# Kernel tuning notes

Measured on AMD Instinct MI355X. Metric: run time of the kernel, lower is better.

## Reference

```python
import jax, jax.numpy as jnp
import numpy as np

N_NODES = 100000
N_EDGES = 640000
N_FEAT = 128


def setup_inputs() -> dict:
    key = jax.random.key(0)
    k1, k2, k3, k4 = jax.random.split(key, 4)
    x = jax.random.normal(k1, (N_NODES, N_FEAT), dtype=jnp.float32)
    edge_index = jax.random.randint(k2, (2, N_EDGES), 0, N_NODES, dtype=jnp.int32)
    # Glorot-ish init for weights
    W_conv = jax.random.normal(k3, (N_FEAT, N_FEAT), dtype=jnp.float32) / np.sqrt(N_FEAT)
    b_conv = jnp.zeros((N_FEAT,), dtype=jnp.float32)
    W_lin = jax.random.normal(k4, (1, N_FEAT), dtype=jnp.float32) / np.sqrt(N_FEAT)
    b_lin = jnp.zeros((1,), dtype=jnp.float32)
    return {"x": x, "edge_index": edge_index, "W_conv": W_conv,
            "b_conv": b_conv, "W_lin": W_lin, "b_lin": b_lin}


def gcn_conv(x, edge_index, W, b):
    # PyG GCNConv: add self-loops, symmetric normalization D^-1/2 (A+I) D^-1/2,
    # linear transform first (no bias in lin), bias added after aggregation.
    N = x.shape[0]
    loop = jnp.arange(N, dtype=edge_index.dtype)
    src = jnp.concatenate([edge_index[0], loop])  # [E+N]
    dst = jnp.concatenate([edge_index[1], loop])  # [E+N]
    deg = jax.ops.segment_sum(jnp.ones_like(dst, dtype=x.dtype), dst, num_segments=N)
    dinv = jnp.where(deg > 0, jax.lax.rsqrt(deg), 0.0)
    norm = dinv[src] * dinv[dst]                   # [E+N]
    xw = x @ W.T                                   # [N, F]
    msg = xw[src] * norm[:, None]                  # [E+N, F] gather + scale
    agg = jax.ops.segment_sum(msg, dst, num_segments=N)  # scatter-add
    return agg + b


def reference(x, edge_index, W_conv, b_conv, W_lin, b_lin):
    h = jax.nn.relu(gcn_conv(x, edge_index, W_conv, b_conv))
    out = jax.nn.sigmoid(h @ W_lin.T + b_lin)
    return (out, h)
```

## Files before the change

### kernel.cpp

```cpp
#include <hip/hip_runtime.h>
#include <hip/hip_bf16.h>

#define NN 100000
#define NE 640000
#define NF 128
#define CAP 32
#define ECAP 36
#define LDW 136
#define EBLK 625
#define XBLK 6250
#define WBLK 8

typedef short bf16x8 __attribute__((ext_vector_type(8)));
typedef float f32x4  __attribute__((ext_vector_type(4)));

__device__ __forceinline__ unsigned short f2bf(float f) {
    union { float f; unsigned int i; } v; v.f = f;
    unsigned int x = v.i;
    return (unsigned short)((x + 0x7FFFu + ((x >> 16) & 1u)) >> 16);
}

__global__ void k_zero(int* __restrict__ fill) {
    int i = blockIdx.x * blockDim.x + threadIdx.x;
    if (i < NN / 4) *(int4*)(fill + i * 4) = (int4){0, 0, 0, 0};
}

__global__ void k_build(const float* __restrict__ x, const float* __restrict__ W,
                        const int* __restrict__ src, const int* __restrict__ dst,
                        int* __restrict__ fill, int* __restrict__ esrc,
                        unsigned short* __restrict__ xs,
                        unsigned short* __restrict__ wb) {
    int b = blockIdx.x;
    if (b < EBLK) {
        int e = (b * 256 + threadIdx.x) * 4;
        int4 s4 = *(const int4*)(src + e);
        int4 d4 = *(const int4*)(dst + e);
        int p0 = atomicAdd(&fill[d4.x], 1);
        int p1 = atomicAdd(&fill[d4.y], 1);
        int p2 = atomicAdd(&fill[d4.z], 1);
        int p3 = atomicAdd(&fill[d4.w], 1);
        if (p0 < CAP) esrc[(long)d4.x * CAP + p0] = s4.x;
        if (p1 < CAP) esrc[(long)d4.y * CAP + p1] = s4.y;
        if (p2 < CAP) esrc[(long)d4.z * CAP + p2] = s4.z;
        if (p3 < CAP) esrc[(long)d4.w * CAP + p3] = s4.w;
    } else if (b < EBLK + XBLK) {
        int t = (b - EBLK) * 256 + threadIdx.x;
        int node = t >> 4, fc = (t & 15) * 8;
        const float* xp = x + (long)node * NF + fc;
        float4 a = *(const float4*)(xp);
        float4 c = *(const float4*)(xp + 4);
        int4 u;
        u.x = (unsigned)f2bf(a.x) | ((unsigned)f2bf(a.y) << 16);
        u.y = (unsigned)f2bf(a.z) | ((unsigned)f2bf(a.w) << 16);
        u.z = (unsigned)f2bf(c.x) | ((unsigned)f2bf(c.y) << 16);
        u.w = (unsigned)f2bf(c.z) | ((unsigned)f2bf(c.w) << 16);
        *(int4*)(xs + (long)node * NF + fc) = u;
    } else {
        int t = (b - EBLK - XBLK) * 256 + threadIdx.x;
        int idx = t * 8;
        float4 a = *(const float4*)(W + idx);
        float4 c = *(const float4*)(W + idx + 4);
        int4 u;
        u.x = (unsigned)f2bf(a.x) | ((unsigned)f2bf(a.y) << 16);
        u.y = (unsigned)f2bf(a.z) | ((unsigned)f2bf(a.w) << 16);
        u.z = (unsigned)f2bf(c.x) | ((unsigned)f2bf(c.y) << 16);
        u.w = (unsigned)f2bf(c.z) | ((unsigned)f2bf(c.w) << 16);
        *(int4*)(wb + idx) = u;
    }
}

__device__ __forceinline__ void acc_row_s(float* acc, int4 u, float s) {
    acc[0] = fmaf(s, __int_as_float((unsigned)u.x << 16), acc[0]);
    acc[1] = fmaf(s, __int_as_float(u.x & 0xffff0000), acc[1]);
    acc[2] = fmaf(s, __int_as_float((unsigned)u.y << 16), acc[2]);
    acc[3] = fmaf(s, __int_as_float(u.y & 0xffff0000), acc[3]);
    acc[4] = fmaf(s, __int_as_float((unsigned)u.z << 16), acc[4]);
    acc[5] = fmaf(s, __int_as_float(u.z & 0xffff0000), acc[5]);
    acc[6] = fmaf(s, __int_as_float((unsigned)u.w << 16), acc[6]);
    acc[7] = fmaf(s, __int_as_float(u.w & 0xffff0000), acc[7]);
}

__launch_bounds__(256, 4)
__global__ void k_fused(const unsigned short* __restrict__ xs,
                        const int* __restrict__ fill,
                        const int* __restrict__ esrc,
                        const unsigned short* __restrict__ wb,
                        const float* __restrict__ bconv,
                        const float* __restrict__ wlin,
                        const float* __restrict__ blin,
                        float* __restrict__ out,
                        float* __restrict__ hout) {
    __shared__ unsigned short lds_a[32 * LDW];
    __shared__ int lds_e[32 * ECAP];
    __shared__ float lds_dv[32];
    __shared__ int lds_dg[32];
    __shared__ float sh_head[2][32];
    int t = threadIdx.x;
    int row0 = blockIdx.x * 32;

    {
        int r = t >> 3, col = (t & 7) * 4;
        *(int4*)(lds_e + r * ECAP + col) =
            *(const int4*)(esrc + (long)(row0 + r) * CAP + col);
    }
    if (t < 32) {
        int dg = fill[row0 + t];
        lds_dv[t] = rsqrtf((float)(dg + 1));
        lds_dg[t] = (dg > CAP) ? CAP : dg;
    }
    __syncthreads();

    {
        int lane = t & 15, slot = t >> 4;
        int fc = lane * 8;
        for (int m = 0; m < 2; ++m) {
            int r = m * 16 + slot;
            int node = row0 + r;
            float dv = lds_dv[r];
            int degc = lds_dg[r];
            const int* ep = lds_e + r * ECAP;

            float acc[8];
            {
                int4 us = *(const int4*)(xs + (long)node * NF + fc);
                acc[0] = dv * __int_as_float((unsigned)us.x << 16);
                acc[1] = dv * __int_as_float(us.x & 0xffff0000);
                acc[2] = dv * __int_as_float((unsigned)us.y << 16);
                acc[3] = dv * __int_as_float(us.y & 0xffff0000);
                acc[4] = dv * __int_as_float((unsigned)us.z << 16);
                acc[5] = dv * __int_as_float(us.z & 0xffff0000);
                acc[6] = dv * __int_as_float((unsigned)us.w << 16);
                acc[7] = dv * __int_as_float(us.w & 0xffff0000);
            }

            for (int j = 0; j < degc; j += 8) {
                int i0 = (j + 0 < degc) ? ep[j + 0] : node;
                int i1 = (j + 1 < degc) ? ep[j + 1] : node;
                int i2 = (j + 2 < degc) ? ep[j + 2] : node;
                int i3 = (j + 3 < degc) ? ep[j + 3] : node;
                int i4 = (j + 4 < degc) ? ep[j + 4] : node;
                int i5 = (j + 5 < degc) ? ep[j + 5] : node;
                int i6 = (j + 6 < degc) ? ep[j + 6] : node;
                int i7 = (j + 7 < degc) ? ep[j + 7] : node;
                int f0 = fill[i0], f1 = fill[i1];
                int f2 = fill[i2], f3 = fill[i3];
                int f4 = fill[i4], f5 = fill[i5];
                int f6 = fill[i6], f7 = fill[i7];
                int4 v0 = *(const int4*)(xs + (long)i0 * NF + fc);
                int4 v1 = *(const int4*)(xs + (long)i1 * NF + fc);
                int4 v2 = *(const int4*)(xs + (long)i2 * NF + fc);
                int4 v3 = *(const int4*)(xs + (long)i3 * NF + fc);
                int4 v4 = *(const int4*)(xs + (long)i4 * NF + fc);
                int4 v5 = *(const int4*)(xs + (long)i5 * NF + fc);
                int4 v6 = *(const int4*)(xs + (long)i6 * NF + fc);
                int4 v7 = *(const int4*)(xs + (long)i7 * NF + fc);
                float s0 = (j + 0 < degc) ? rsqrtf((float)(f0 + 1)) : 0.f;
                float s1 = (j + 1 < degc) ? rsqrtf((float)(f1 + 1)) : 0.f;
                float s2 = (j + 2 < degc) ? rsqrtf((float)(f2 + 1)) : 0.f;
                float s3 = (j + 3 < degc) ? rsqrtf((float)(f3 + 1)) : 0.f;
                float s4 = (j + 4 < degc) ? rsqrtf((float)(f4 + 1)) : 0.f;
                float s5 = (j + 5 < degc) ? rsqrtf((float)(f5 + 1)) : 0.f;
                float s6 = (j + 6 < degc) ? rsqrtf((float)(f6 + 1)) : 0.f;
                float s7 = (j + 7 < degc) ? rsqrtf((float)(f7 + 1)) : 0.f;
                acc_row_s(acc, v0, s0); acc_row_s(acc, v1, s1);
                acc_row_s(acc, v2, s2); acc_row_s(acc, v3, s3);
                acc_row_s(acc, v4, s4); acc_row_s(acc, v5, s5);
                acc_row_s(acc, v6, s6); acc_row_s(acc, v7, s7);
            }

            int4 st;
            st.x = (unsigned)f2bf(acc[0] * dv) | ((unsigned)f2bf(acc[1] * dv) << 16);
            st.y = (unsigned)f2bf(acc[2] * dv) | ((unsigned)f2bf(acc[3] * dv) << 16);
            st.z = (unsigned)f2bf(acc[4] * dv) | ((unsigned)f2bf(acc[5] * dv) << 16);
            st.w = (unsigned)f2bf(acc[6] * dv) | ((unsigned)f2bf(acc[7] * dv) << 16);
            *(int4*)(lds_a + r * LDW + fc) = st;
        }
    }
    __syncthreads();

    int w = t >> 6, lane = t & 63;
    int quad = lane >> 4, nr = lane & 15;
    int mrow = (w >> 1) * 16;
    int ncol0 = (w & 1) * 64;
    int kq = quad * 8;

    f32x4 acc4[4];
#pragma unroll
    for (int nt = 0; nt < 4; ++nt) acc4[nt] = (f32x4){0.f, 0.f, 0.f, 0.f};

#pragma unroll
    for (int ks = 0; ks < 4; ++ks) {
        bf16x8 af = *(const bf16x8*)(lds_a + (mrow + nr) * LDW + ks * 32 + kq);
#pragma unroll
        for (int nt = 0; nt < 4; ++nt) {
            bf16x8 bf = *(const bf16x8*)(wb + (ncol0 + nt * 16 + nr) * NF + ks * 32 + kq);
            acc4[nt] = __builtin_amdgcn_mfma_f32_16x16x32_bf16(af, bf, acc4[nt], 0, 0, 0);
        }
    }

    float bcv[4], wlv[4];
#pragma unroll
    for (int nt = 0; nt < 4; ++nt) {
        int col = ncol0 + nt * 16 + nr;
        bcv[nt] = bconv[col];
        wlv[nt] = wlin[col];
    }
    float p[4] = {0.f, 0.f, 0.f, 0.f};
#pragma unroll
    for (int nt = 0; nt < 4; ++nt) {
        int col = ncol0 + nt * 16 + nr;
#pragma unroll
        for (int r = 0; r < 4; ++r) {
            float h = fmaxf(acc4[nt][r] + bcv[nt], 0.0f);
            int row = row0 + mrow + quad * 4 + r;
            hout[(long)row * NF + col] = h;
            p[r] += h * wlv[nt];
        }
    }
#pragma unroll
    for (int r = 0; r < 4; ++r) {
#pragma unroll
        for (int off = 1; off <= 8; off <<= 1)
            p[r] += __shfl_xor(p[r], off, 64);
        if (nr == 0) sh_head[w & 1][mrow + quad * 4 + r] = p[r];
    }
    __syncthreads();
    if (t < 32) {
        float z = sh_head[0][t] + sh_head[1][t] + blin[0];
        out[row0 + t] = 1.0f / (1.0f + expf(-z));
    }
}

extern "C" void kernel_launch(void* const* d_in, const int* in_sizes, int n_in,
                              void* d_out, int out_size, void* d_ws, size_t ws_size,
                              hipStream_t stream) {
    const float* x     = (const float*)d_in[0];
    const int*   ei    = (const int*)d_in[1];
    const float* Wc    = (const float*)d_in[2];
    const float* bconv = (const float*)d_in[3];
    const float* wlin  = (const float*)d_in[4];
    const float* blin  = (const float*)d_in[5];
    const int* src = ei;
    const int* dst = ei + NE;

    float* out  = (float*)d_out;
    float* hout = out + NN;

    int*            esrc = (int*)d_ws;
    unsigned short* xs   = (unsigned short*)(esrc + (size_t)NN * CAP);
    unsigned short* wb   = xs + (size_t)NN * NF;
    int*            fill = (int*)(wb + NF * NF);

    k_zero <<<(NN / 4 + 255) / 256, 256, 0, stream>>>(fill);
    k_build<<<EBLK + XBLK + WBLK, 256, 0, stream>>>(x, Wc, src, dst,
                                                    fill, esrc, xs, wb);
    k_fused<<<NN / 32, 256, 0, stream>>>(xs, fill, esrc, wb,
                                         bconv, wlin, blin, out, hout);
}
```

Before: 200.9 us.

## Transform features before aggregation; fuse GEMM into build and epilogue into aggregation

The linear transform now runs before aggregation, matching the reference order. The bf16 MFMA GEMM moves into the build kernel, where it runs alongside the edge-bucketing atomics and writes bf16 pre-activations. The aggregation kernel then gathers those transformed rows and applies bias, ReLU, the output head and the sigmoid per row, which removes the LDS staging and the second barrier-heavy GEMM phase. The zero and W-convert steps merge into one init kernel, and edge bucketing goes to one edge per thread. Rounding x@W to bf16 before the sum changes the numerics slightly.

```diff
diff --git a/kernel.cpp b/kernel.cpp
--- a/kernel.cpp
+++ b/kernel.cpp
@@ -7,9 +7,9 @@
 #define CAP 32
 #define ECAP 36
 #define LDW 136
-#define EBLK 625
-#define XBLK 6250
-#define WBLK 8
+#define ABLK 2500
+#define NTILE 3125
+#define NN_PAD 100352
 
 typedef short bf16x8 __attribute__((ext_vector_type(8)));
 typedef float f32x4  __attribute__((ext_vector_type(4)));
@@ -19,44 +19,16 @@
     unsigned int x = v.i;
     return (unsigned short)((x + 0x7FFFu + ((x >> 16) & 1u)) >> 16);
 }
-
-__global__ void k_zero(int* __restrict__ fill) {
-    int i = blockIdx.x * blockDim.x + threadIdx.x;
-    if (i < NN / 4) *(int4*)(fill + i * 4) = (int4){0, 0, 0, 0};
-}
-
-__global__ void k_build(const float* __restrict__ x, const float* __restrict__ W,
-                        const int* __restrict__ src, const int* __restrict__ dst,
-                        int* __restrict__ fill, int* __restrict__ esrc,
-                        unsigned short* __restrict__ xs,
-                        unsigned short* __restrict__ wb) {
-    int b = blockIdx.x;
-    if (b < EBLK) {
-        int e = (b * 256 + threadIdx.x) * 4;
-        int4 s4 = *(const int4*)(src + e);
-        int4 d4 = *(const int4*)(dst + e);
-        int p0 = atomicAdd(&fill[d4.x], 1);
-        int p1 = atomicAdd(&fill[d4.y], 1);
-        int p2 = atomicAdd(&fill[d4.z], 1);
-        int p3 = atomicAdd(&fill[d4.w], 1);
-        if (p0 < CAP) esrc[(long)d4.x * CAP + p0] = s4.x;
-        if (p1 < CAP) esrc[(long)d4.y * CAP + p1] = s4.y;
-        if (p2 < CAP) esrc[(long)d4.z * CAP + p2] = s4.z;
-        if (p3 < CAP) esrc[(long)d4.w * CAP + p3] = s4.w;
-    } else if (b < EBLK + XBLK) {
-        int t = (b - EBLK) * 256 + threadIdx.x;
-        int node = t >> 4, fc = (t & 15) * 8;
-        const float* xp = x + (long)node * NF + fc;
-        float4 a = *(const float4*)(xp);
-        float4 c = *(const float4*)(xp + 4);
-        int4 u;
-        u.x = (unsigned)f2bf(a.x) | ((unsigned)f2bf(a.y) << 16);
-        u.y = (unsigned)f2bf(a.z) | ((unsigned)f2bf(a.w) << 16);
-        u.z = (unsigned)f2bf(c.x) | ((unsigned)f2bf(c.y) << 16);
-        u.w = (unsigned)f2bf(c.z) | ((unsigned)f2bf(c.w) << 16);
-        *(int4*)(xs + (long)node * NF + fc) = u;
+__device__ __forceinline__ float bflo(int u) { return __int_as_float((unsigned)u << 16); }
+__device__ __forceinline__ float bfhi(int u) { return __int_as_float(u & 0xffff0000); }
+
+__global__ void k_init(const float* __restrict__ W, int* __restrict__ fill,
+                       unsigned short* __restrict__ wb) {
+    int i = blockIdx.x * 256 + threadIdx.x;
+    if (i < NN_PAD / 4) {
+        *(int4*)(fill + i * 4) = (int4){0, 0, 0, 0};
     } else {
-        int t = (b - EBLK - XBLK) * 256 + threadIdx.x;
+        int t = i - NN_PAD / 4;
         int idx = t * 8;
         float4 a = *(const float4*)(W + idx);
         float4 c = *(const float4*)(W + idx + 4);
@@ -69,32 +41,81 @@
     }
 }
 
-__device__ __forceinline__ void acc_row_s(float* acc, int4 u, float s) {
-    acc[0] = fmaf(s, __int_as_float((unsigned)u.x << 16), acc[0]);
-    acc[1] = fmaf(s, __int_as_float(u.x & 0xffff0000), acc[1]);
-    acc[2] = fmaf(s, __int_as_float((unsigned)u.y << 16), acc[2]);
-    acc[3] = fmaf(s, __int_as_float(u.y & 0xffff0000), acc[3]);
-    acc[4] = fmaf(s, __int_as_float((unsigned)u.z << 16), acc[4]);
-    acc[5] = fmaf(s, __int_as_float(u.z & 0xffff0000), acc[5]);
-    acc[6] = fmaf(s, __int_as_float((unsigned)u.w << 16), acc[6]);
-    acc[7] = fmaf(s, __int_as_float(u.w & 0xffff0000), acc[7]);
-}
-
 __launch_bounds__(256, 4)
-__global__ void k_fused(const unsigned short* __restrict__ xs,
-                        const int* __restrict__ fill,
-                        const int* __restrict__ esrc,
+__global__ void k_build(const float* __restrict__ x,
+                        const int* __restrict__ src, const int* __restrict__ dst,
+                        int* __restrict__ fill, int* __restrict__ esrc,
                         const unsigned short* __restrict__ wb,
-                        const float* __restrict__ bconv,
-                        const float* __restrict__ wlin,
-                        const float* __restrict__ blin,
-                        float* __restrict__ out,
-                        float* __restrict__ hout) {
+                        unsigned short* __restrict__ hpre) {
     __shared__ unsigned short lds_a[32 * LDW];
+    int bid = blockIdx.x, t = threadIdx.x;
+
+    if (bid < ABLK) {
+        int e = bid * 256 + t;
+        int s = src[e], d = dst[e];
+        int pos = atomicAdd(&fill[d], 1);
+        if (pos < CAP) esrc[(long)d * CAP + pos] = s;
+        return;
+    }
+
+    int row0 = (bid - ABLK) * 32;
+    {
+        int r = t >> 3, cb = (t & 7) * 16;
+        const float* xp = x + (long)(row0 + r) * NF + cb;
+        float4 a = *(const float4*)(xp);
+        float4 b = *(const float4*)(xp + 4);
+        float4 c = *(const float4*)(xp + 8);
+        float4 d = *(const float4*)(xp + 12);
+        int4 u1, u2;
+        u1.x = (unsigned)f2bf(a.x) | ((unsigned)f2bf(a.y) << 16);
+        u1.y = (unsigned)f2bf(a.z) | ((unsigned)f2bf(a.w) << 16);
+        u1.z = (unsigned)f2bf(b.x) | ((unsigned)f2bf(b.y) << 16);
+        u1.w = (unsigned)f2bf(b.z) | ((unsigned)f2bf(b.w) << 16);
+        u2.x = (unsigned)f2bf(c.x) | ((unsigned)f2bf(c.y) << 16);
+        u2.y = (unsigned)f2bf(c.z) | ((unsigned)f2bf(c.w) << 16);
+        u2.z = (unsigned)f2bf(d.x) | ((unsigned)f2bf(d.y) << 16);
+        u2.w = (unsigned)f2bf(d.z) | ((unsigned)f2bf(d.w) << 16);
+        *(int4*)(lds_a + r * LDW + cb) = u1;
+        *(int4*)(lds_a + r * LDW + cb + 8) = u2;
+    }
+    __syncthreads();
+
+    int w = t >> 6, lane = t & 63;
+    int quad = lane >> 4, nr = lane & 15;
+    int mrow = (w >> 1) * 16, ncol0 = (w & 1) * 64, kq = quad * 8;
+
+    f32x4 acc4[4];
+#pragma unroll
+    for (int nt = 0; nt < 4; ++nt) acc4[nt] = (f32x4){0.f, 0.f, 0.f, 0.f};
+#pragma unroll
+    for (int ks = 0; ks < 4; ++ks) {
+        bf16x8 af = *(const bf16x8*)(lds_a + (mrow + nr) * LDW + ks * 32 + kq);
+#pragma unroll
+        for (int nt = 0; nt < 4; ++nt) {
+            bf16x8 bfr = *(const bf16x8*)(wb + (ncol0 + nt * 16 + nr) * NF + ks * 32 + kq);
+            acc4[nt] = __builtin_amdgcn_mfma_f32_16x16x32_bf16(af, bfr, acc4[nt], 0, 0, 0);
+        }
+    }
+#pragma unroll
+    for (int nt = 0; nt < 4; ++nt) {
+        int col = ncol0 + nt * 16 + nr;
+#pragma unroll
+        for (int g = 0; g < 4; ++g)
+            hpre[(long)(row0 + mrow + quad * 4 + g) * NF + col] = f2bf(acc4[nt][g]);
+    }
+}
+
+__launch_bounds__(256, 4)
+__global__ void k_agg(const unsigned short* __restrict__ hpre,
+                      const int* __restrict__ fill,
+                      const int* __restrict__ esrc,
+                      const float* __restrict__ bconv,
+                      const float* __restrict__ wlin,
+                      const float* __restrict__ blin,
+                      float* __restrict__ out, float* __restrict__ hout) {
     __shared__ int lds_e[32 * ECAP];
     __shared__ float lds_dv[32];
     __shared__ int lds_dg[32];
-    __shared__ float sh_head[2][32];
     int t = threadIdx.x;
     int row0 = blockIdx.x * 32;
 
@@ -110,124 +131,108 @@
     }
     __syncthreads();
 
-    {
-        int lane = t & 15, slot = t >> 4;
-        int fc = lane * 8;
-        for (int m = 0; m < 2; ++m) {
-            int r = m * 16 + slot;
-            int node = row0 + r;
-            float dv = lds_dv[r];
-            int degc = lds_dg[r];
-            const int* ep = lds_e + r * ECAP;
-
-            float acc[8];
-            {
-                int4 us = *(const int4*)(xs + (long)node * NF + fc);
-                acc[0] = dv * __int_as_float((unsigned)us.x << 16);
-                acc[1] = dv * __int_as_float(us.x & 0xffff0000);
-                acc[2] = dv * __int_as_float((unsigned)us.y << 16);
-                acc[3] = dv * __int_as_float(us.y & 0xffff0000);
-                acc[4] = dv * __int_as_float((unsigned)us.z << 16);
-                acc[5] = dv * __int_as_float(us.z & 0xffff0000);
-                acc[6] = dv * __int_as_float((unsigned)us.w << 16);
-                acc[7] = dv * __int_as_float(us.w & 0xffff0000);
-            }
-
-            for (int j = 0; j < degc; j += 8) {
-                int i0 = (j + 0 < degc) ? ep[j + 0] : node;
-                int i1 = (j + 1 < degc) ? ep[j + 1] : node;
-                int i2 = (j + 2 < degc) ? ep[j + 2] : node;
-                int i3 = (j + 3 < degc) ? ep[j + 3] : node;
-                int i4 = (j + 4 < degc) ? ep[j + 4] : node;
-                int i5 = (j + 5 < degc) ? ep[j + 5] : node;
-                int i6 = (j + 6 < degc) ? ep[j + 6] : node;
-                int i7 = (j + 7 < degc) ? ep[j + 7] : node;
-                int f0 = fill[i0], f1 = fill[i1];
-                int f2 = fill[i2], f3 = fill[i3];
-                int f4 = fill[i4], f5 = fill[i5];
-                int f6 = fill[i6], f7 = fill[i7];
-                int4 v0 = *(const int4*)(xs + (long)i0 * NF + fc);
-                int4 v1 = *(const int4*)(xs + (long)i1 * NF + fc);
-                int4 v2 = *(const int4*)(xs + (long)i2 * NF + fc);
-                int4 v3 = *(const int4*)(xs + (long)i3 * NF + fc);
-                int4 v4 = *(const int4*)(xs + (long)i4 * NF + fc);
-                int4 v5 = *(const int4*)(xs + (long)i5 * NF + fc);
-                int4 v6 = *(const int4*)(xs + (long)i6 * NF + fc);
-                int4 v7 = *(const int4*)(xs + (long)i7 * NF + fc);
-                float s0 = (j + 0 < degc) ? rsqrtf((float)(f0 + 1)) : 0.f;
-                float s1 = (j + 1 < degc) ? rsqrtf((float)(f1 + 1)) : 0.f;
-                float s2 = (j + 2 < degc) ? rsqrtf((float)(f2 + 1)) : 0.f;
-                float s3 = (j + 3 < degc) ? rsqrtf((float)(f3 + 1)) : 0.f;
-                float s4 = (j + 4 < degc) ? rsqrtf((float)(f4 + 1)) : 0.f;
-                float s5 = (j + 5 < degc) ? rsqrtf((float)(f5 + 1)) : 0.f;
-                float s6 = (j + 6 < degc) ? rsqrtf((float)(f6 + 1)) : 0.f;
-                float s7 = (j + 7 < degc) ? rsqrtf((float)(f7 + 1)) : 0.f;
-                acc_row_s(acc, v0, s0); acc_row_s(acc, v1, s1);
-                acc_row_s(acc, v2, s2); acc_row_s(acc, v3, s3);
-                acc_row_s(acc, v4, s4); acc_row_s(acc, v5, s5);
-                acc_row_s(acc, v6, s6); acc_row_s(acc, v7, s7);
-            }
-
-            int4 st;
-            st.x = (unsigned)f2bf(acc[0] * dv) | ((unsigned)f2bf(acc[1] * dv) << 16);
-            st.y = (unsigned)f2bf(acc[2] * dv) | ((unsigned)f2bf(acc[3] * dv) << 16);
-            st.z = (unsigned)f2bf(acc[4] * dv) | ((unsigned)f2bf(acc[5] * dv) << 16);
-            st.w = (unsigned)f2bf(acc[6] * dv) | ((unsigned)f2bf(acc[7] * dv) << 16);
-            *(int4*)(lds_a + r * LDW + fc) = st;
+    int lane = t & 15, slot = t >> 4;
+    int fc = lane * 8;
+    float bl = blin[0];
+
+    for (int m = 0; m < 2; ++m) {
+        int r = m * 16 + slot;
+        int node = row0 + r;
+        float dv = lds_dv[r];
+        int degc = lds_dg[r];
+        const int* ep = lds_e + r * ECAP;
+
+        float acc[8];
+        {
+            int4 us = *(const int4*)(hpre + (long)node * NF + fc);
+            acc[0] = dv * bflo(us.x); acc[1] = dv * bfhi(us.x);
+            acc[2] = dv * bflo(us.y); acc[3] = dv * bfhi(us.y);
+            acc[4] = dv * bflo(us.z); acc[5] = dv * bfhi(us.z);
+            acc[6] = dv * bflo(us.w); acc[7] = dv * bfhi(us.w);
         }
-    }
-    __syncthreads();
-
-    int w = t >> 6, lane = t & 63;
-    int quad = lane >> 4, nr = lane & 15;
-    int mrow = (w >> 1) * 16;
-    int ncol0 = (w & 1) * 64;
-    int kq = quad * 8;
-
-    f32x4 acc4[4];
-#pragma unroll
-    for (int nt = 0; nt < 4; ++nt) acc4[nt] = (f32x4){0.f, 0.f, 0.f, 0.f};
-
-#pragma unroll
-    for (int ks = 0; ks < 4; ++ks) {
-        bf16x8 af = *(const bf16x8*)(lds_a + (mrow + nr) * LDW + ks * 32 + kq);
-#pragma unroll
-        for (int nt = 0; nt < 4; ++nt) {
-            bf16x8 bf = *(const bf16x8*)(wb + (ncol0 + nt * 16 + nr) * NF + ks * 32 + kq);
-            acc4[nt] = __builtin_amdgcn_mfma_f32_16x16x32_bf16(af, bf, acc4[nt], 0, 0, 0);
+        for (int j = 0; j < degc; j += 8) {
+            int i0 = (j + 0 < degc) ? ep[j + 0] : node;
+            int i1 = (j + 1 < degc) ? ep[j + 1] : node;
+            int i2 = (j + 2 < degc) ? ep[j + 2] : node;
+            int i3 = (j + 3 < degc) ? ep[j + 3] : node;
+            int i4 = (j + 4 < degc) ? ep[j + 4] : node;
+            int i5 = (j + 5 < degc) ? ep[j + 5] : node;
+            int i6 = (j + 6 < degc) ? ep[j + 6] : node;
+            int i7 = (j + 7 < degc) ? ep[j + 7] : node;
+            int f0 = fill[i0], f1 = fill[i1], f2 = fill[i2], f3 = fill[i3];
+            int f4 = fill[i4], f5 = fill[i5], f6 = fill[i6], f7 = fill[i7];
+            int4 v0 = *(const int4*)(hpre + (long)i0 * NF + fc);
+            int4 v1 = *(const int4*)(hpre + (long)i1 * NF + fc);
+            int4 v2 = *(const int4*)(hpre + (long)i2 * NF + fc);
+            int4 v3 = *(const int4*)(hpre + (long)i3 * NF + fc);
+            int4 v4 = *(const int4*)(hpre + (long)i4 * NF + fc);
+            int4 v5 = *(const int4*)(hpre + (long)i5 * NF + fc);
+            int4 v6 = *(const int4*)(hpre + (long)i6 * NF + fc);
+            int4 v7 = *(const int4*)(hpre + (long)i7 * NF + fc);
+            float s0 = (j + 0 < degc) ? rsqrtf((float)(f0 + 1)) : 0.f;
+            float s1 = (j + 1 < degc) ? rsqrtf((float)(f1 + 1)) : 0.f;
+            float s2 = (j + 2 < degc) ? rsqrtf((float)(f2 + 1)) : 0.f;
+            float s3 = (j + 3 < degc) ? rsqrtf((float)(f3 + 1)) : 0.f;
+            float s4 = (j + 4 < degc) ? rsqrtf((float)(f4 + 1)) : 0.f;
+            float s5 = (j + 5 < degc) ? rsqrtf((float)(f5 + 1)) : 0.f;
+            float s6 = (j + 6 < degc) ? rsqrtf((float)(f6 + 1)) : 0.f;
+            float s7 = (j + 7 < degc) ? rsqrtf((float)(f7 + 1)) : 0.f;
+            acc[0] = fmaf(s0, bflo(v0.x), acc[0]); acc[1] = fmaf(s0, bfhi(v0.x), acc[1]);
+            acc[2] = fmaf(s0, bflo(v0.y), acc[2]); acc[3] = fmaf(s0, bfhi(v0.y), acc[3]);
+            acc[4] = fmaf(s0, bflo(v0.z), acc[4]); acc[5] = fmaf(s0, bfhi(v0.z), acc[5]);
+            acc[6] = fmaf(s0, bflo(v0.w), acc[6]); acc[7] = fmaf(s0, bfhi(v0.w), acc[7]);
+            acc[0] = fmaf(s1, bflo(v1.x), acc[0]); acc[1] = fmaf(s1, bfhi(v1.x), acc[1]);
+            acc[2] = fmaf(s1, bflo(v1.y), acc[2]); acc[3] = fmaf(s1, bfhi(v1.y), acc[3]);
+            acc[4] = fmaf(s1, bflo(v1.z), acc[4]); acc[5] = fmaf(s1, bfhi(v1.z), acc[5]);
+            acc[6] = fmaf(s1, bflo(v1.w), acc[6]); acc[7] = fmaf(s1, bfhi(v1.w), acc[7]);
+            acc[0] = fmaf(s2, bflo(v2.x), acc[0]); acc[1] = fmaf(s2, bfhi(v2.x), acc[1]);
+            acc[2] = fmaf(s2, bflo(v2.y), acc[2]); acc[3] = fmaf(s2, bfhi(v2.y), acc[3]);
+            acc[4] = fmaf(s2, bflo(v2.z), acc[4]); acc[5] = fmaf(s2, bfhi(v2.z), acc[5]);
+            acc[6] = fmaf(s2, bflo(v2.w), acc[6]); acc[7] = fmaf(s2, bfhi(v2.w), acc[7]);
+            acc[0] = fmaf(s3, bflo(v3.x), acc[0]); acc[1] = fmaf(s3, bfhi(v3.x), acc[1]);
+            acc[2] = fmaf(s3, bflo(v3.y), acc[2]); acc[3] = fmaf(s3, bfhi(v3.y), acc[3]);
+            acc[4] = fmaf(s3, bflo(v3.z), acc[4]); acc[5] = fmaf(s3, bfhi(v3.z), acc[5]);
+            acc[6] = fmaf(s3, bflo(v3.w), acc[6]); acc[7] = fmaf(s3, bfhi(v3.w), acc[7]);
+            acc[0] = fmaf(s4, bflo(v4.x), acc[0]); acc[1] = fmaf(s4, bfhi(v4.x), acc[1]);
+            acc[2] = fmaf(s4, bflo(v4.y), acc[2]); acc[3] = fmaf(s4, bfhi(v4.y), acc[3]);
+            acc[4] = fmaf(s4, bflo(v4.z), acc[4]); acc[5] = fmaf(s4, bfhi(v4.z), acc[5]);
+            acc[6] = fmaf(s4, bflo(v4.w), acc[6]); acc[7] = fmaf(s4, bfhi(v4.w), acc[7]);
+            acc[0] = fmaf(s5, bflo(v5.x), acc[0]); acc[1] = fmaf(s5, bfhi(v5.x), acc[1]);
+            acc[2] = fmaf(s5, bflo(v5.y), acc[2]); acc[3] = fmaf(s5, bfhi(v5.y), acc[3]);
+            acc[4] = fmaf(s5, bflo(v5.z), acc[4]); acc[5] = fmaf(s5, bfhi(v5.z), acc[5]);
+            acc[6] = fmaf(s5, bflo(v5.w), acc[6]); acc[7] = fmaf(s5, bfhi(v5.w), acc[7]);
+            acc[0] = fmaf(s6, bflo(v6.x), acc[0]); acc[1] = fmaf(s6, bfhi(v6.x), acc[1]);
+            acc[2] = fmaf(s6, bflo(v6.y), acc[2]); acc[3] = fmaf(s6, bfhi(v6.y), acc[3]);
+            acc[4] = fmaf(s6, bflo(v6.z), acc[4]); acc[5] = fmaf(s6, bfhi(v6.z), acc[5]);
+            acc[6] = fmaf(s6, bflo(v6.w), acc[6]); acc[7] = fmaf(s6, bfhi(v6.w), acc[7]);
+            acc[0] = fmaf(s7, bflo(v7.x), acc[0]); acc[1] = fmaf(s7, bfhi(v7.x), acc[1]);
+            acc[2] = fmaf(s7, bflo(v7.y), acc[2]); acc[3] = fmaf(s7, bfhi(v7.y), acc[3]);
+            acc[4] = fmaf(s7, bflo(v7.z), acc[4]); acc[5] = fmaf(s7, bfhi(v7.z), acc[5]);
+            acc[6] = fmaf(s7, bflo(v7.w), acc[6]); acc[7] = fmaf(s7, bfhi(v7.w), acc[7]);
         }
-    }
-
-    float bcv[4], wlv[4];
-#pragma unroll
-    for (int nt = 0; nt < 4; ++nt) {
-        int col = ncol0 + nt * 16 + nr;
-        bcv[nt] = bconv[col];
-        wlv[nt] = wlin[col];
-    }
-    float p[4] = {0.f, 0.f, 0.f, 0.f};
-#pragma unroll
-    for (int nt = 0; nt < 4; ++nt) {
-        int col = ncol0 + nt * 16 + nr;
-#pragma unroll
-        for (int r = 0; r < 4; ++r) {
-            float h = fmaxf(acc4[nt][r] + bcv[nt], 0.0f);
-            int row = row0 + mrow + quad * 4 + r;
-            hout[(long)row * NF + col] = h;
-            p[r] += h * wlv[nt];
-        }
-    }
-#pragma unroll
-    for (int r = 0; r < 4; ++r) {
+
+        float4 bc0 = *(const float4*)(bconv + fc);
+        float4 bc1 = *(const float4*)(bconv + fc + 4);
+        float4 wl0 = *(const float4*)(wlin + fc);
+        float4 wl1 = *(const float4*)(wlin + fc + 4);
+        float4 h0, h1;
+        h0.x = fmaxf(acc[0] * dv + bc0.x, 0.f);
+        h0.y = fmaxf(acc[1] * dv + bc0.y, 0.f);
+        h0.z = fmaxf(acc[2] * dv + bc0.z, 0.f);
+        h0.w = fmaxf(acc[3] * dv + bc0.w, 0.f);
+        h1.x = fmaxf(acc[4] * dv + bc1.x, 0.f);
+        h1.y = fmaxf(acc[5] * dv + bc1.y, 0.f);
+        h1.z = fmaxf(acc[6] * dv + bc1.z, 0.f);
+        h1.w = fmaxf(acc[7] * dv + bc1.w, 0.f);
+        *(float4*)(hout + (long)node * NF + fc) = h0;
+        *(float4*)(hout + (long)node * NF + fc + 4) = h1;
+        float p = h0.x * wl0.x + h0.y * wl0.y + h0.z * wl0.z + h0.w * wl0.w
+                + h1.x * wl1.x + h1.y * wl1.y + h1.z * wl1.z + h1.w * wl1.w;
 #pragma unroll
         for (int off = 1; off <= 8; off <<= 1)
-            p[r] += __shfl_xor(p[r], off, 64);
-        if (nr == 0) sh_head[w & 1][mrow + quad * 4 + r] = p[r];
-    }
-    __syncthreads();
-    if (t < 32) {
-        float z = sh_head[0][t] + sh_head[1][t] + blin[0];
-        out[row0 + t] = 1.0f / (1.0f + expf(-z));
+            p += __shfl_xor(p, off, 64);
+        if (lane == 0)
+            out[node] = 1.0f / (1.0f + expf(-(p + bl)));
     }
 }
 
@@ -247,13 +252,11 @@
     float* hout = out + NN;
 
     int*            esrc = (int*)d_ws;
-    unsigned short* xs   = (unsigned short*)(esrc + (size_t)NN * CAP);
-    unsigned short* wb   = xs + (size_t)NN * NF;
+    unsigned short* hpre = (unsigned short*)(esrc + (size_t)NN * CAP);
+    unsigned short* wb   = hpre + (size_t)NN * NF;
     int*            fill = (int*)(wb + NF * NF);
-
-    k_zero <<<(NN / 4 + 255) / 256, 256, 0, stream>>>(fill);
-    k_build<<<EBLK + XBLK + WBLK, 256, 0, stream>>>(x, Wc, src, dst,
-                                                    fill, esrc, xs, wb);
-    k_fused<<<NN / 32, 256, 0, stream>>>(xs, fill, esrc, wb,
-                                         bconv, wlin, blin, out, hout);
-}
+    
+    k_init <<<106, 256, 0, stream>>>(Wc, fill, wb);
+    k_build<<<ABLK + NTILE, 256, 0, stream>>>(x, src, dst, fill, esrc, wb, hpre);
+    k_agg  <<<NTILE, 256, 0, stream>>>(hpre, fill, esrc, bconv, wlin, blin, out, hout);
+}
```

New measurement: 192.1 us. -4.4%, faster.
